# Kernel optimization log

Hardware: AMD Instinct MI355X
Metric: run time of the kernel (lower is better)

## Reference

```python
import jax, jax.numpy as jnp
import numpy as np

B, C_IN, H, W_IN = 32, 128, 64, 64
C_OUT, K = 256, 3


def setup_inputs() -> dict:
    key = jax.random.key(0)
    kx, kw = jax.random.split(key)
    x = jax.random.normal(kx, (B, C_IN, H, W_IN), dtype=jnp.float32)
    # original initializes weights as binary {0,1} floats
    W = jax.random.randint(kw, (C_OUT, C_IN, K, K), 0, 2).astype(jnp.float32)
    return {"x": x, "W": W}


def reference(x, W):
    # XOR-style conv: out[b,co,ho,wo] = sum(patch * (1 - 2*W[co]))
    # stride=1, padding=0 (hardcoded in the original forward).
    eff_w = 1.0 - 2.0 * W  # (C_OUT, C_IN, K, K)
    return jax.lax.conv_general_dilated(
        x, eff_w,
        window_strides=(1, 1),
        padding='VALID',
        dimension_numbers=('NCHW', 'OIHW', 'NCHW'),
    )
```

## Files before the change

### kernel.cpp

```cpp
#include <hip/hip_runtime.h>


typedef __bf16 bf16x8 __attribute__((ext_vector_type(8)));
typedef float  f32x4  __attribute__((ext_vector_type(4)));

#define CIPAD 40

__global__ void prepack_w_kernel(const float* __restrict__ Wf,
                                 unsigned short* __restrict__ effw) {
  int idx = blockIdx.x * 256 + threadIdx.x;
  if (idx >= 9 * 4 * 16 * 64 * 8) return;
  int j    = idx & 7;
  int lane = (idx >> 3) & 63;
  int tile = (idx >> 9) & 15;
  int cc   = (idx >> 13) & 3;
  int e    = idx >> 15;
  int co = tile * 16 + (lane & 15);
  int ci = cc * 32 + (lane >> 4) * 8 + j;
  float w = Wf[(co * 128 + ci) * 9 + e];
  __bf16 h = (__bf16)(1.0f - 2.0f * w);
  unsigned short u; __builtin_memcpy(&u, &h, 2);
  effw[idx] = u;
}

__global__ __launch_bounds__(256, 2)
void xorconv_mfma_kernel(const float* __restrict__ x,
                         const unsigned short* __restrict__ effw,
                         float* __restrict__ out) {
  __shared__ __align__(16) unsigned short xs[6 * 66 * CIPAD];

  const int tid    = threadIdx.x;
  const int bxc    = blockIdx.x;
  const int co_blk = bxc * 128;
  const int hbase  = blockIdx.y * 4;
  const int bb     = blockIdx.z;

  const int wv   = tid >> 6;
  const int lane = tid & 63;
  const int quad = lane >> 4;
  const int l16  = lane & 15;

  f32x4 acc[8][4];
  #pragma unroll
  for (int i = 0; i < 8; ++i)
    #pragma unroll
    for (int j = 0; j < 4; ++j)
      acc[i][j] = (f32x4){0.f, 0.f, 0.f, 0.f};

  unsigned int* xs32 = (unsigned int*)xs;

  for (int cc = 0; cc < 4; ++cc) {
    const int c0 = cc * 32;

    for (int p2 = tid; p2 < 6 * 33 * 16; p2 += 256) {
      int c2  = p2 % 33;
      int t2  = p2 / 33;
      int ci2 = t2 & 15;
      int r   = t2 >> 4;
      int c   = c2 * 2;
      int h_in = hbase + r; if (h_in > 63) h_in = 63;
      int c_in = c;         if (c_in > 62) c_in = 62;
      const float* gp = x + (((size_t)(bb * 128 + c0 + ci2 * 2) * 64 + h_in) * 64 + c_in);
      float f00 = gp[0],    f01 = gp[1];
      float f10 = gp[4096], f11 = gp[4097];
      __bf16 h00 = (__bf16)f00, h01 = (__bf16)f01, h10 = (__bf16)f10, h11 = (__bf16)f11;
      unsigned short u00, u01, u10, u11;
      __builtin_memcpy(&u00, &h00, 2); __builtin_memcpy(&u01, &h01, 2);
      __builtin_memcpy(&u10, &h10, 2); __builtin_memcpy(&u11, &h11, 2);
      xs32[(r * 66 + c) * (CIPAD / 2) + ci2]     = (unsigned)u00 | ((unsigned)u10 << 16);
      xs32[(r * 66 + c + 1) * (CIPAD / 2) + ci2] = (unsigned)u01 | ((unsigned)u11 << 16);
    }
    __syncthreads();

    for (int e = 0; e < 9; ++e) {
      const int kh = e / 3;
      const int kw = e - 3 * kh;
      const int rr = wv + kh;

      bf16x8 bfr[4];
      #pragma unroll
      for (int j = 0; j < 4; ++j) {
        int ccol = j * 16 + l16 + kw;
        bfr[j] = *(const bf16x8*)&xs[(rr * 66 + ccol) * CIPAD + quad * 8];
      }
      const unsigned short* wp =
          effw + ((((size_t)e * 4 + cc) * 16 + bxc * 8) * 64 + lane) * 8;
      #pragma unroll
      for (int mt = 0; mt < 8; ++mt) {
        bf16x8 af = *(const bf16x8*)(wp + (size_t)mt * 512);
        #pragma unroll
        for (int j = 0; j < 4; ++j)
          acc[mt][j] = __builtin_amdgcn_mfma_f32_16x16x32_bf16(af, bfr[j], acc[mt][j], 0, 0, 0);
      }
    }
    __syncthreads();
  }

  const int ho = hbase + wv;
  if (ho < 62) {
    #pragma unroll
    for (int mt = 0; mt < 8; ++mt) {
      const int co = co_blk + mt * 16 + quad * 4;
      #pragma unroll
      for (int j = 0; j < 4; ++j) {
        const int wo = j * 16 + l16;
        if (wo < 62) {
          float* op = out + (((size_t)(bb * 256 + co) * 62 + ho) * 62 + wo);
          #pragma unroll
          for (int rg = 0; rg < 4; ++rg)
            op[(size_t)rg * 3844] = acc[mt][j][rg];
        }
      }
    }
  }
}

extern "C" void kernel_launch(void* const* d_in, const int* in_sizes, int n_in,
                              void* d_out, int out_size, void* d_ws, size_t ws_size,
                              hipStream_t stream) {
  const float* x  = (const float*)d_in[0];
  const float* Wf = (const float*)d_in[1];
  float* out = (float*)d_out;
  unsigned short* effw = (unsigned short*)d_ws;

  prepack_w_kernel<<<dim3((9 * 4 * 16 * 64 * 8 + 255) / 256), dim3(256), 0, stream>>>(Wf, effw);

  dim3 grid(2, 16, 32);
  xorconv_mfma_kernel<<<grid, dim3(256), 0, stream>>>(x, effw, out);
}
```

Before: 284.0 us.

## Prepack input to bf16 channel-interleaved layout in a separate kernel

Adds a pre-pass kernel that converts x to bf16 and reorders it into a [b][h][cc][col][32 ci] layout in workspace, so the conv kernel can fill shared memory with contiguous 16-byte vector loads. The goal is to remove the strided fp32 gathers and per-element conversions that were repeated by both channel-out blocks in the main kernel. In exchange it adds an extra kernel launch plus a full read of x and a write and re-read of a 32 MB bf16 copy. The old path is kept as a fallback when the workspace is too small.

```diff
diff --git a/kernel.cpp b/kernel.cpp
--- a/kernel.cpp
+++ b/kernel.cpp
@@ -23,10 +23,31 @@
   effw[idx] = u;
 }
 
+__global__ void prepack_x_kernel(const float* __restrict__ x,
+                                 unsigned short* __restrict__ xbf) {
+  int t = blockIdx.x * 256 + threadIdx.x;
+  if (t >= 32 * 64 * 4 * 4 * 64) return;
+  int c  = t & 63;
+  int q  = (t >> 6) & 3;
+  int cc = (t >> 8) & 3;
+  int h  = (t >> 10) & 63;
+  int b  = t >> 16;
+  int ci0 = cc * 32 + q * 8;
+  unsigned short u[8];
+  #pragma unroll
+  for (int j = 0; j < 8; ++j) {
+    float f = x[((size_t)(b * 128 + ci0 + j) * 64 + h) * 64 + c];
+    __bf16 hh = (__bf16)f;
+    __builtin_memcpy(&u[j], &hh, 2);
+  }
+  size_t idx = ((((size_t)(b * 64 + h) * 4 + cc) * 64 + c) * 32) + q * 8;
+  *(uint4*)&xbf[idx] = *(const uint4*)u;
+}
+
 __global__ __launch_bounds__(256, 2)
-void xorconv_mfma_kernel(const float* __restrict__ x,
-                         const unsigned short* __restrict__ effw,
-                         float* __restrict__ out) {
+void xorconv_mfma_pre(const unsigned short* __restrict__ xbf,
+                      const unsigned short* __restrict__ effw,
+                      float* __restrict__ out) {
   __shared__ __align__(16) unsigned short xs[6 * 66 * CIPAD];
 
   const int tid    = threadIdx.x;
@@ -40,6 +61,9 @@
   const int quad = lane >> 4;
   const int l16  = lane & 15;
 
+  const int qst = tid & 3;
+  const int cst = (tid >> 2) & 63;
+
   f32x4 acc[8][4];
   #pragma unroll
   for (int i = 0; i < 8; ++i)
@@ -47,11 +71,89 @@
     for (int j = 0; j < 4; ++j)
       acc[i][j] = (f32x4){0.f, 0.f, 0.f, 0.f};
 
+  for (int cc = 0; cc < 4; ++cc) {
+    uint4 v[6];
+    #pragma unroll
+    for (int r = 0; r < 6; ++r) {
+      int h_in = hbase + r; if (h_in > 63) h_in = 63;
+      const unsigned short* sp =
+          xbf + ((((size_t)(bb * 64 + h_in) * 4 + cc) * 64 + cst) * 32) + qst * 8;
+      v[r] = *(const uint4*)sp;
+    }
+    #pragma unroll
+    for (int r = 0; r < 6; ++r)
+      *(uint4*)&xs[(r * 66 + cst) * CIPAD + qst * 8] = v[r];
+    __syncthreads();
+
+    for (int e = 0; e < 9; ++e) {
+      const int kh = e / 3;
+      const int kw = e - 3 * kh;
+      const int rr = wv + kh;
+
+      bf16x8 bfr[4];
+      #pragma unroll
+      for (int j = 0; j < 4; ++j) {
+        int ccol = j * 16 + l16 + kw;
+        bfr[j] = *(const bf16x8*)&xs[(rr * 66 + ccol) * CIPAD + quad * 8];
+      }
+      const unsigned short* wp =
+          effw + ((((size_t)e * 4 + cc) * 16 + bxc * 8) * 64 + lane) * 8;
+      #pragma unroll
+      for (int mt = 0; mt < 8; ++mt) {
+        bf16x8 af = *(const bf16x8*)(wp + (size_t)mt * 512);
+        #pragma unroll
+        for (int j = 0; j < 4; ++j)
+          acc[mt][j] = __builtin_amdgcn_mfma_f32_16x16x32_bf16(af, bfr[j], acc[mt][j], 0, 0, 0);
+      }
+    }
+    __syncthreads();
+  }
+
+  const int ho = hbase + wv;
+  if (ho < 62) {
+    #pragma unroll
+    for (int mt = 0; mt < 8; ++mt) {
+      const int co = co_blk + mt * 16 + quad * 4;
+      #pragma unroll
+      for (int j = 0; j < 4; ++j) {
+        const int wo = j * 16 + l16;
+        if (wo < 62) {
+          float* op = out + (((size_t)(bb * 256 + co) * 62 + ho) * 62 + wo);
+          #pragma unroll
+          for (int rg = 0; rg < 4; ++rg)
+            op[(size_t)rg * 3844] = acc[mt][j][rg];
+        }
+      }
+    }
+  }
+}
+
+__global__ __launch_bounds__(256, 2)
+void xorconv_mfma_fb(const float* __restrict__ x,
+                     const unsigned short* __restrict__ effw,
+                     float* __restrict__ out) {
+  __shared__ __align__(16) unsigned short xs[6 * 66 * CIPAD];
+  const int tid    = threadIdx.x;
+  const int bxc    = blockIdx.x;
+  const int co_blk = bxc * 128;
+  const int hbase  = blockIdx.y * 4;
+  const int bb     = blockIdx.z;
+  const int wv   = tid >> 6;
+  const int lane = tid & 63;
+  const int quad = lane >> 4;
+  const int l16  = lane & 15;
+
+  f32x4 acc[8][4];
+  #pragma unroll
+  for (int i = 0; i < 8; ++i)
+    #pragma unroll
+    for (int j = 0; j < 4; ++j)
+      acc[i][j] = (f32x4){0.f, 0.f, 0.f, 0.f};
+
   unsigned int* xs32 = (unsigned int*)xs;
 
   for (int cc = 0; cc < 4; ++cc) {
     const int c0 = cc * 32;
-
     for (int p2 = tid; p2 < 6 * 33 * 16; p2 += 256) {
       int c2  = p2 % 33;
       int t2  = p2 / 33;
@@ -71,12 +173,10 @@
       xs32[(r * 66 + c + 1) * (CIPAD / 2) + ci2] = (unsigned)u01 | ((unsigned)u11 << 16);
     }
     __syncthreads();
-
     for (int e = 0; e < 9; ++e) {
       const int kh = e / 3;
       const int kw = e - 3 * kh;
       const int rr = wv + kh;
-
       bf16x8 bfr[4];
       #pragma unroll
       for (int j = 0; j < 4; ++j) {
@@ -121,10 +221,19 @@
   const float* x  = (const float*)d_in[0];
   const float* Wf = (const float*)d_in[1];
   float* out = (float*)d_out;
+
   unsigned short* effw = (unsigned short*)d_ws;
+  const size_t XBF_OFF = 2u * 1024u * 1024u;
+  const size_t XBF_BYTES = (size_t)32 * 64 * 4 * 64 * 32 * 2;
+  unsigned short* xbf = (unsigned short*)((char*)d_ws + XBF_OFF);
 
   prepack_w_kernel<<<dim3((9 * 4 * 16 * 64 * 8 + 255) / 256), dim3(256), 0, stream>>>(Wf, effw);
 
   dim3 grid(2, 16, 32);
-  xorconv_mfma_kernel<<<grid, dim3(256), 0, stream>>>(x, effw, out);
-}
+  if (ws_size >= XBF_OFF + XBF_BYTES) {
+    prepack_x_kernel<<<dim3(2097152 / 256), dim3(256), 0, stream>>>(x, xbf);
+    xorconv_mfma_pre<<<grid, dim3(256), 0, stream>>>(xbf, effw, out);
+  } else {
+    xorconv_mfma_fb<<<grid, dim3(256), 0, stream>>>(x, effw, out);
+  }
+}
```

After: 308.5 us. 1.09x slower.
